# Optimization experiments

Hardware: AMD Instinct MI355X
Metric: run time of the kernel (lower is better)

## Reference

```python
import jax, jax.numpy as jnp
import numpy as np

N_NODES = 20000
N_EDGES = 640000
C_IN = 128      # num_node_features
K_FOLDS = 8     # num_edge_features
FILTERS = 128


def setup_inputs() -> dict:
    key = jax.random.key(0)
    k1, k2, k3, k4, k5, k6 = jax.random.split(key, 6)
    node_features = jax.random.normal(k1, (N_NODES, C_IN), dtype=jnp.float32)
    edge_features = jax.random.uniform(k2, (K_FOLDS, N_EDGES), dtype=jnp.float32)
    rows = jax.random.randint(k3, (N_EDGES,), 0, N_NODES)
    cols = jax.random.randint(k4, (N_EDGES,), 0, N_NODES)
    indices = jnp.stack([rows, cols], axis=1).astype(jnp.int64)
    # glorot_uniform kernel [K, C_in, filters]
    limit = np.sqrt(6.0 / (C_IN + FILTERS))
    kernel = jax.random.uniform(k5, (K_FOLDS, C_IN, FILTERS), dtype=jnp.float32,
                                minval=-limit, maxval=limit)
    bias = jnp.zeros((FILTERS,), dtype=jnp.float32)
    return {
        "node_features": node_features,
        "edge_features": edge_features,
        "kernel": kernel,
        "bias": bias,
        "indices": indices,
        "out_size": N_NODES,
    }


def reference(node_features, edge_features, kernel, bias, indices, out_size):
    # fold_conv: out[i,f] = sum_{e: row(e)=i} sum_k ef[k,e] * (x[col(e)] @ kernel[k])[f]
    row = indices[:, 0]
    col = indices[:, 1]
    xg = node_features[col]  # [E, C] gathered source-node features
    E = xg.shape[0]
    msgs = jnp.zeros((E, kernel.shape[2]), dtype=node_features.dtype)
    # Loop over the small fixed number of folds (K=8); each iteration is a
    # dense [E,C]x[C,F] matmul scaled by the per-edge fold weight.
    for k in range(kernel.shape[0]):
        msgs = msgs + (xg @ kernel[k]) * edge_features[k][:, None]
    out = jax.ops.segment_sum(msgs, row, num_segments=out_size)  # [out_size, F]
    out = out + bias  # bias_add; activation is None (linear)
    return out
```

## Files before the change

kernel.cpp:

```cpp
#include <hip/hip_runtime.h>
#include <cstddef>
#include <cstdint>

static constexpr int kNodes   = 20000;
static constexpr int kEdges   = 640000;
static constexpr int kCin     = 128;
static constexpr int kFolds   = 8;
static constexpr int kFilters = 128;
static constexpr int kKdim    = kFolds * kCin;
static constexpr int kCap     = 80;

static constexpr int kNBucket = 250;
static constexpr int kRowsPB  = 80;
static constexpr int kCapB    = 3072;
static constexpr int kBin1Blk = 160;

typedef __attribute__((ext_vector_type(8))) short v8s;
typedef __attribute__((ext_vector_type(4))) float v4f;

__device__ __forceinline__ unsigned short f2bf(float f) {
    union { float f; uint32_t u; } v; v.f = f;
    const uint32_t u = v.u;
    return (unsigned short)((u + 0x7fffu + ((u >> 16) & 1u)) >> 16);
}
__device__ __forceinline__ float bf2f(unsigned short s) {
    union { uint32_t u; float f; } v; v.u = ((uint32_t)s) << 16;
    return v.f;
}

__global__ __launch_bounds__(256) void prep_k(
    const int2*  __restrict__ idx2,
    const float* __restrict__ ef,
    const float* __restrict__ x,
    const float* __restrict__ W,
    int* __restrict__ bucketCnt,
    int2* __restrict__ pairs,
    unsigned int* __restrict__ rec,
    unsigned short* __restrict__ xb,
    unsigned short* __restrict__ Wt)
{
    const int b = blockIdx.x;
    const int t = threadIdx.x;
    if (b < 2500) {
        const int e = b * 256 + t;
        const int2 rc = idx2[e];
        union { uint4 q; unsigned int w[4]; unsigned short s[8]; } o;
        #pragma unroll
        for (int k = 0; k < kFolds; ++k)
            o.s[k] = f2bf(ef[(size_t)k * kEdges + e]);
        uint4* recp = (uint4*)(rec + (size_t)e * 8);
        recp[0] = make_uint4((unsigned)rc.y, o.w[0], o.w[1], o.w[2]);
        recp[1] = make_uint4(o.w[3], 0u, 0u, 0u);
    } else if (b < 3750) {
        const int i = (b - 2500) * 2048 + t * 8;
        const float4 a = *(const float4*)(x + i);
        const float4 c = *(const float4*)(x + i + 4);
        union { uint4 q; unsigned short s[8]; } o;
        o.s[0] = f2bf(a.x); o.s[1] = f2bf(a.y); o.s[2] = f2bf(a.z); o.s[3] = f2bf(a.w);
        o.s[4] = f2bf(c.x); o.s[5] = f2bf(c.y); o.s[6] = f2bf(c.z); o.s[7] = f2bf(c.w);
        *(uint4*)(xb + i) = o.q;
    } else if (b < 3814) {
        const int t2 = (b - 3750) * 256 + t;
        const int n  = t2 & 127;
        const int k8 = t2 >> 7;
        union { uint4 q; unsigned short s[8]; } o;
        #pragma unroll
        for (int j = 0; j < 8; ++j)
            o.s[j] = f2bf(W[(size_t)(k8 * 8 + j) * kFilters + n]);
        *(uint4*)(Wt + (size_t)n * kKdim + k8 * 8) = o.q;
    } else {
        __shared__ int hist[kNBucket];
        __shared__ int base[kNBucket];
        const int bb = b - 3814;
        const int e0 = bb * 4096;

        if (t < kNBucket) hist[t] = 0;
        __syncthreads();

        int rowsReg[16];
        #pragma unroll
        for (int i = 0; i < 16; ++i) {
            const int e = e0 + i * 256 + t;
            int row = -1;
            if (e < kEdges) {
                row = idx2[e].x;
                atomicAdd(&hist[row / kRowsPB], 1);
            }
            rowsReg[i] = row;
        }
        __syncthreads();

        if (t < kNBucket) {
            const int h = hist[t];
            base[t] = atomicAdd(&bucketCnt[t], h);
            hist[t] = 0;
        }
        __syncthreads();

        #pragma unroll
        for (int i = 0; i < 16; ++i) {
            const int row = rowsReg[i];
            if (row >= 0) {
                const int e  = e0 + i * 256 + t;
                const int bk = row / kRowsPB;
                const int sl = base[bk] + atomicAdd(&hist[bk], 1);
                if (sl < kCapB)
                    pairs[(size_t)bk * kCapB + sl] = make_int2(row, e);
            }
        }
    }
}

__global__ __launch_bounds__(256) void bin2_k(
    const int2* __restrict__ pairs,
    const int*  __restrict__ bucketCnt,
    int* __restrict__ ebuf,
    int* __restrict__ cnt)
{
    __shared__ int c80[kRowsPB];
    const int b = blockIdx.x;
    const int t = threadIdx.x;

    if (t < kRowsPB) c80[t] = 0;
    __syncthreads();

    int n = bucketCnt[b];
    n = n < kCapB ? n : kCapB;
    const int2* seg = pairs + (size_t)b * kCapB;

    for (int s = t; s < n; s += 256) {
        const int2 p = seg[s];
        const int rl = p.x - b * kRowsPB;
        const int c  = atomicAdd(&c80[rl], 1);
        if (c < kCap) ebuf[p.x * kCap + c] = p.y;
    }
    __syncthreads();

    if (t < kRowsPB) cnt[b * kRowsPB + t] = c80[t];
}

__global__ __launch_bounds__(64) void pull_k(
    const unsigned short* __restrict__ xb,
    const int*  __restrict__ ebuf,
    const unsigned int* __restrict__ rec,
    const int*  __restrict__ cnt,
    unsigned short* __restrict__ S)
{
    __shared__ int   sCol[4][kCap];
    __shared__ float sEf[4][kCap][8];
    __shared__ int   sDeg[4];

    const int t  = threadIdx.x;
    const int n0 = blockIdx.x * 4;

    if (t < 4) {
        int d = cnt[n0 + t];
        sDeg[t] = d < kCap ? d : kCap;
    }
    #pragma unroll
    for (int gg = 0; gg < 4; ++gg) {
        const int nn = n0 + gg;
        int dg = cnt[nn];
        dg = dg < kCap ? dg : kCap;
        for (int s = t; s < dg; s += 64) {
            const int e = ebuf[nn * kCap + s];
            const uint4 q0   = *(const uint4*)(rec + (size_t)e * 8);
            const unsigned w3 = rec[(size_t)e * 8 + 4];
            sCol[gg][s] = (int)q0.x;
            sEf[gg][s][0] = bf2f((unsigned short)(q0.y));
            sEf[gg][s][1] = bf2f((unsigned short)(q0.y >> 16));
            sEf[gg][s][2] = bf2f((unsigned short)(q0.z));
            sEf[gg][s][3] = bf2f((unsigned short)(q0.z >> 16));
            sEf[gg][s][4] = bf2f((unsigned short)(q0.w));
            sEf[gg][s][5] = bf2f((unsigned short)(q0.w >> 16));
            sEf[gg][s][6] = bf2f((unsigned short)(w3));
            sEf[gg][s][7] = bf2f((unsigned short)(w3 >> 16));
        }
    }
    __syncthreads();

    const int g  = t >> 4;
    const int c8 = (t & 15) * 8;
    const int n  = n0 + g;
    const int deg = sDeg[g];

    float acc[8][8];
    #pragma unroll
    for (int k = 0; k < 8; ++k)
        #pragma unroll
        for (int j = 0; j < 8; ++j) acc[k][j] = 0.f;

    const unsigned short* xbase = xb + c8;
    v8s xcur;
    if (deg > 0) xcur = *(const v8s*)(xbase + (size_t)sCol[g][0] * kCin);

    for (int i = 0; i < deg; ++i) {
        const int nidx = (i + 1 < deg) ? i + 1 : i;
        const v8s xnext = *(const v8s*)(xbase + (size_t)sCol[g][nidx] * kCin);

        float xf[8];
        #pragma unroll
        for (int j = 0; j < 8; ++j) xf[j] = bf2f((unsigned short)xcur[j]);

        const float4 wa = *(const float4*)&sEf[g][i][0];
        const float4 wc = *(const float4*)&sEf[g][i][4];
        const float w[8] = {wa.x, wa.y, wa.z, wa.w, wc.x, wc.y, wc.z, wc.w};

        #pragma unroll
        for (int k = 0; k < 8; ++k)
            #pragma unroll
            for (int j = 0; j < 8; ++j)
                acc[k][j] += w[k] * xf[j];

        xcur = xnext;
    }

    unsigned short* srow = S + (size_t)n * kKdim + c8;
    #pragma unroll
    for (int k = 0; k < 8; ++k) {
        union { uint4 q; unsigned short s[8]; } o;
        #pragma unroll
        for (int j = 0; j < 8; ++j) o.s[j] = f2bf(acc[k][j]);
        *(uint4*)(srow + k * kCin) = o.q;
    }
}

static constexpr int BM  = 64;
static constexpr int BK  = 32;
static constexpr int SWS = 40;

__global__ __launch_bounds__(256) void gemm_k(
    const unsigned short* __restrict__ S,
    const unsigned short* __restrict__ Wt,
    const float* __restrict__ bias,
    float* __restrict__ out)
{
    __shared__ unsigned short sS[BM * SWS];
    __shared__ unsigned short sWt[kFilters * SWS];

    const int t    = threadIdx.x;
    const int wave = t >> 6;
    const int lane = t & 63;
    const int quad = lane >> 4;
    const int r16  = lane & 15;
    const int m0   = blockIdx.x * BM;

    v4f acc[8];
    #pragma unroll
    for (int i = 0; i < 8; ++i) acc[i] = (v4f){0.f, 0.f, 0.f, 0.f};

    for (int k0 = 0; k0 < kKdim; k0 += BK) {
        {
            const int row = t >> 2;
            const int kc  = (t & 3) * 8;
            const int m   = m0 + row;
            uint4 v = make_uint4(0, 0, 0, 0);
            if (m < kNodes)
                v = *(const uint4*)(S + (size_t)m * kKdim + k0 + kc);
            *(uint4*)&sS[row * SWS + kc] = v;
        }
        {
            const int n    = t >> 1;
            const int half = (t & 1) * 16;
            const unsigned short* src = Wt + (size_t)n * kKdim + k0 + half;
            *(uint4*)&sWt[n * SWS + half]     = *(const uint4*)(src);
            *(uint4*)&sWt[n * SWS + half + 8] = *(const uint4*)(src + 8);
        }
        __syncthreads();

        const v8s a = *(const v8s*)&sS[(wave * 16 + r16) * SWS + quad * 8];
        #pragma unroll
        for (int nt = 0; nt < 8; ++nt) {
            const v8s b = *(const v8s*)&sWt[(nt * 16 + r16) * SWS + quad * 8];
            acc[nt] = __builtin_amdgcn_mfma_f32_16x16x32_bf16(a, b, acc[nt], 0, 0, 0);
        }
        __syncthreads();
    }

    #pragma unroll
    for (int nt = 0; nt < 8; ++nt) {
        const int n = nt * 16 + r16;
        const float bv = bias[n];
        #pragma unroll
        for (int r = 0; r < 4; ++r) {
            const int m = m0 + wave * 16 + quad * 4 + r;
            if (m < kNodes)
                out[(size_t)m * kFilters + n] = acc[nt][r] + bv;
        }
    }
}

extern "C" void kernel_launch(void* const* d_in, const int* in_sizes, int n_in,
                              void* d_out, int out_size, void* d_ws, size_t ws_size,
                              hipStream_t stream) {
    const float* x    = (const float*)d_in[0];
    const float* ef   = (const float*)d_in[1];
    const float* W    = (const float*)d_in[2];
    const float* bias = (const float*)d_in[3];
    const int2*  idx2 = (const int2*)d_in[4];
    float* out = (float*)d_out;

    char* ws = (char*)d_ws;
    unsigned short* S      = (unsigned short*)(ws);
    int2*           pairs  = (int2*)(ws);
    unsigned int*   rec    = (unsigned int*)(ws + 40960000);
    int*            ebuf   = (int*)(ws + 61440000);
    unsigned short* xb     = (unsigned short*)(ws + 67840000);
    unsigned short* Wt     = (unsigned short*)(ws + 72960000);
    int*            cnt    = (int*)(ws + 73222144);
    int*            bucketCnt = (int*)(ws + 73302144);

    hipMemsetAsync(bucketCnt, 0, kNBucket * sizeof(int), stream);

    prep_k<<<3814 + kBin1Blk, 256, 0, stream>>>(idx2, ef, x, W, bucketCnt,
                                                pairs, rec, xb, Wt);
    bin2_k<<<kNBucket, 256, 0, stream>>>(pairs, bucketCnt, ebuf, cnt);
    pull_k<<<kNodes / 4, 64, 0, stream>>>(xb, ebuf, rec, cnt, S);
    gemm_k<<<(kNodes + BM - 1) / BM, 256, 0, stream>>>(S, Wt, bias, out);
}
```

Baseline: 185.4 us.

## Split each node's edge list across two half-waves and deepen gather prefetch

The pull kernel now handles 8 nodes per 256-thread block. Each node gets 32 lanes, and its edges are split by parity between two 16-lane halves, whose partial accumulators are combined with a cross-lane shuffle. Edge weights stay packed as bf16 in shared memory. Each thread prefetches four neighbor rows at a time instead of one, with the edge list zero-padded to a multiple of 8. The aim is more memory-level parallelism and shorter per-thread serial chains in the gather, at the cost of padded dummy work and the shuffle reduction.

```diff
diff --git a/kernel.cpp b/kernel.cpp
--- a/kernel.cpp
+++ b/kernel.cpp
@@ -25,6 +25,14 @@
 }
 __device__ __forceinline__ float bf2f(unsigned short s) {
     union { uint32_t u; float f; } v; v.u = ((uint32_t)s) << 16;
+    return v.f;
+}
+__device__ __forceinline__ float bflo(unsigned int u) {
+    union { uint32_t u; float f; } v; v.u = u << 16;
+    return v.f;
+}
+__device__ __forceinline__ float bfhi(unsigned int u) {
+    union { uint32_t u; float f; } v; v.u = u & 0xFFFF0000u;
     return v.f;
 }
 
@@ -139,50 +147,54 @@
     if (t < kRowsPB) cnt[b * kRowsPB + t] = c80[t];
 }
 
-__global__ __launch_bounds__(64) void pull_k(
+__global__ __launch_bounds__(256, 4) void pull_k(
     const unsigned short* __restrict__ xb,
     const int*  __restrict__ ebuf,
     const unsigned int* __restrict__ rec,
     const int*  __restrict__ cnt,
     unsigned short* __restrict__ S)
 {
-    __shared__ int   sCol[4][kCap];
-    __shared__ float sEf[4][kCap][8];
-    __shared__ int   sDeg[4];
+    __shared__ int          sCol[8][kCap];
+    __shared__ unsigned int sEf[8][kCap][4];
+    __shared__ int          sDeg[8];
 
     const int t  = threadIdx.x;
-    const int n0 = blockIdx.x * 4;
-
-    if (t < 4) {
-        int d = cnt[n0 + t];
-        sDeg[t] = d < kCap ? d : kCap;
-    }
-    #pragma unroll
-    for (int gg = 0; gg < 4; ++gg) {
-        const int nn = n0 + gg;
+    const int n0 = blockIdx.x * 8;
+
+    {
+        const int g8 = t >> 5;
+        const int s0 = t & 31;
+        const int nn = n0 + g8;
         int dg = cnt[nn];
         dg = dg < kCap ? dg : kCap;
-        for (int s = t; s < dg; s += 64) {
+        const int dgP = (dg + 7) & ~7;
+        for (int s = s0; s < dg; s += 32) {
             const int e = ebuf[nn * kCap + s];
-            const uint4 q0   = *(const uint4*)(rec + (size_t)e * 8);
+            const uint4 q0    = *(const uint4*)(rec + (size_t)e * 8);
             const unsigned w3 = rec[(size_t)e * 8 + 4];
-            sCol[gg][s] = (int)q0.x;
-            sEf[gg][s][0] = bf2f((unsigned short)(q0.y));
-            sEf[gg][s][1] = bf2f((unsigned short)(q0.y >> 16));
-            sEf[gg][s][2] = bf2f((unsigned short)(q0.z));
-            sEf[gg][s][3] = bf2f((unsigned short)(q0.z >> 16));
-            sEf[gg][s][4] = bf2f((unsigned short)(q0.w));
-            sEf[gg][s][5] = bf2f((unsigned short)(q0.w >> 16));
-            sEf[gg][s][6] = bf2f((unsigned short)(w3));
-            sEf[gg][s][7] = bf2f((unsigned short)(w3 >> 16));
-        }
+            sCol[g8][s] = (int)q0.x;
+            *(uint4*)&sEf[g8][s][0] = make_uint4(q0.y, q0.z, q0.w, w3);
+        }
+        for (int s = dg + s0; s < dgP; s += 32) {
+            sCol[g8][s] = 0;
+            *(uint4*)&sEf[g8][s][0] = make_uint4(0u, 0u, 0u, 0u);
+        }
+        if (s0 == 0) sDeg[g8] = dg;
     }
     __syncthreads();
 
-    const int g  = t >> 4;
-    const int c8 = (t & 15) * 8;
-    const int n  = n0 + g;
-    const int deg = sDeg[g];
+    const int wave = t >> 6;
+    const int lane = t & 63;
+    const int g    = lane >> 5;
+    const int h    = (lane >> 4) & 1;
+    const int r    = lane & 15;
+    const int ln   = wave * 2 + g;
+    const int node = n0 + ln;
+    const int c8   = r * 8;
+
+    const int deg  = sDeg[ln];
+    const int degP = (deg + 7) & ~7;
+    const int half = degP >> 1;
 
     float acc[8][8];
     #pragma unroll
@@ -191,33 +203,55 @@
         for (int j = 0; j < 8; ++j) acc[k][j] = 0.f;
 
     const unsigned short* xbase = xb + c8;
-    v8s xcur;
-    if (deg > 0) xcur = *(const v8s*)(xbase + (size_t)sCol[g][0] * kCin);
-
-    for (int i = 0; i < deg; ++i) {
-        const int nidx = (i + 1 < deg) ? i + 1 : i;
-        const v8s xnext = *(const v8s*)(xbase + (size_t)sCol[g][nidx] * kCin);
-
+
+    auto proc = [&](v8s xv, int i) {
         float xf[8];
         #pragma unroll
-        for (int j = 0; j < 8; ++j) xf[j] = bf2f((unsigned short)xcur[j]);
-
-        const float4 wa = *(const float4*)&sEf[g][i][0];
-        const float4 wc = *(const float4*)&sEf[g][i][4];
-        const float w[8] = {wa.x, wa.y, wa.z, wa.w, wc.x, wc.y, wc.z, wc.w};
-
+        for (int jj = 0; jj < 8; ++jj) xf[jj] = bf2f((unsigned short)xv[jj]);
+        const uint4 ew = *(const uint4*)&sEf[ln][i][0];
+        float w8[8];
+        w8[0] = bflo(ew.x); w8[1] = bfhi(ew.x);
+        w8[2] = bflo(ew.y); w8[3] = bfhi(ew.y);
+        w8[4] = bflo(ew.z); w8[5] = bfhi(ew.z);
+        w8[6] = bflo(ew.w); w8[7] = bfhi(ew.w);
         #pragma unroll
         for (int k = 0; k < 8; ++k)
             #pragma unroll
-            for (int j = 0; j < 8; ++j)
-                acc[k][j] += w[k] * xf[j];
-
-        xcur = xnext;
-    }
-
-    unsigned short* srow = S + (size_t)n * kKdim + c8;
-    #pragma unroll
-    for (int k = 0; k < 8; ++k) {
+            for (int jj = 0; jj < 8; ++jj)
+                acc[k][jj] += w8[k] * xf[jj];
+    };
+
+    v8s x0 = (v8s)0, x1 = (v8s)0, x2 = (v8s)0, x3 = (v8s)0;
+    if (half > 0) {
+        x0 = *(const v8s*)(xbase + (size_t)sCol[ln][h]     * kCin);
+        x1 = *(const v8s*)(xbase + (size_t)sCol[ln][h + 2] * kCin);
+        x2 = *(const v8s*)(xbase + (size_t)sCol[ln][h + 4] * kCin);
+        x3 = *(const v8s*)(xbase + (size_t)sCol[ln][h + 6] * kCin);
+    }
+
+    for (int j = 0; j < half; j += 4) {
+        const int nj = (j + 4 < half) ? (j + 4) : j;
+        const v8s y0 = *(const v8s*)(xbase + (size_t)sCol[ln][2*nj     + h] * kCin);
+        const v8s y1 = *(const v8s*)(xbase + (size_t)sCol[ln][2*(nj+1) + h] * kCin);
+        const v8s y2 = *(const v8s*)(xbase + (size_t)sCol[ln][2*(nj+2) + h] * kCin);
+        const v8s y3 = *(const v8s*)(xbase + (size_t)sCol[ln][2*(nj+3) + h] * kCin);
+
+        proc(x0, 2*j + h); proc(x1, 2*(j+1) + h);
+        proc(x2, 2*(j+2) + h); proc(x3, 2*(j+3) + h);
+
+        x0 = y0; x1 = y1; x2 = y2; x3 = y3;
+    }
+
+    #pragma unroll
+    for (int k = 0; k < 8; ++k)
+        #pragma unroll
+        for (int j = 0; j < 8; ++j)
+            acc[k][j] += __shfl_xor(acc[k][j], 16);
+
+    unsigned short* srow = S + (size_t)node * kKdim + c8;
+    #pragma unroll
+    for (int kk = 0; kk < 4; ++kk) {
+        const int k = h * 4 + kk;
         union { uint4 q; unsigned short s[8]; } o;
         #pragma unroll
         for (int j = 0; j < 8; ++j) o.s[j] = f2bf(acc[k][j]);
@@ -315,6 +349,6 @@
     prep_k<<<3814 + kBin1Blk, 256, 0, stream>>>(idx2, ef, x, W, bucketCnt,
                                                 pairs, rec, xb, Wt);
     bin2_k<<<kNBucket, 256, 0, stream>>>(pairs, bucketCnt, ebuf, cnt);
-    pull_k<<<kNodes / 4, 64, 0, stream>>>(xb, ebuf, rec, cnt, S);
+    pull_k<<<kNodes / 8, 256, 0, stream>>>(xb, ebuf, rec, cnt, S);
     gemm_k<<<(kNodes + BM - 1) / BM, 256, 0, stream>>>(S, Wt, bias, out);
 }
```

After: 313.2 us. 1.69x slower.
